# Kernel optimization log

Measured on AMD Instinct MI355X. Metric: run time of the kernel, lower is better.

Reference implementation:

```python
import jax, jax.numpy as jnp
import numpy as np

NEG = -1e6  # matches torch masked value of -1000000.0
EPS = 1e-5


def setup_inputs() -> dict:
    key = jax.random.key(0)
    k1, k2, k3, k4, k5, k6 = jax.random.split(key, 6)
    B, H, L, D = 2, 16, 2048, 128
    BH = B * H
    return {
        "queries": jax.random.normal(k1, (BH, L, D), dtype=jnp.float32),
        "keys": jax.random.normal(k2, (BH, L, D), dtype=jnp.float32),
        "values": jax.random.normal(k3, (BH, L, D), dtype=jnp.float32),
        "q_mult": jax.random.normal(k4, (B, L, D), dtype=jnp.float32),
        "kv_mult": jax.random.normal(k5, (B, L, D), dtype=jnp.float32),
        "valid_lens": jax.random.randint(k6, (BH,), 0, L, dtype=jnp.int64),
        "num_heads": 16,
    }


def reference(queries, keys, values, q_mult, kv_mult, valid_lens, num_heads):
    # queries/keys/values: [BH, L, d]; q_mult/kv_mult: [B, L, d_m]; valid_lens: [BH]
    d = queries.shape[-1]
    Lk = keys.shape[1]
    scale = 1.0 / jnp.sqrt(jnp.asarray(d, dtype=queries.dtype))
    scores = jnp.einsum('bqd,bkd->bqk', queries, keys) * scale  # [BH, Lq, Lk]

    # custom additive multiplicative-interaction term, Frobenius-normalized per batch element
    mult_ = jnp.einsum('bqd,bkd->bqk', q_mult, kv_mult)  # [B, Lq, Lk]
    fro = jnp.sqrt(jnp.sum(mult_ * mult_, axis=(1, 2), keepdims=True))
    mult_ = mult_ / (fro + EPS)
    mult_ = jnp.repeat(mult_, num_heads, axis=0)  # [BH, Lq, Lk]

    # masked softmax over keys: valid_lens is per-(batch*head), broadcast over queries
    key_mask = jnp.arange(Lk)[None, None, :] < valid_lens[:, None, None]  # [BH, 1, Lk]
    scores = jnp.where(key_mask, scores, NEG)
    attn = jax.nn.softmax(scores, axis=-1) + mult_  # after_softmax=True path

    # dropout is identity (p=0 / eval)
    return jnp.einsum('bqk,bkd->bqd', attn, values)
```

## Files before the change

### kernel.cpp

```cpp
#include <hip/hip_runtime.h>


typedef __attribute__((ext_vector_type(8))) __bf16 bf16x8;
typedef __attribute__((ext_vector_type(16))) float f32x16;
typedef __attribute__((ext_vector_type(4))) unsigned int u32x4;

#define DEV static __device__ __forceinline__

constexpr int LL = 2048, DD = 128, BH = 32;
constexpr float SCALE = 0.08838834764831845f;
constexpr float SCALE2 = 0.12752736105f;
constexpr float NEGV = -1e6f;

DEV unsigned pkb(float a, float b) {
  union { __bf16 h[2]; unsigned u; } x;
  x.h[0] = (__bf16)a; x.h[1] = (__bf16)b;
  return x.u;
}
DEV f32x16 mfma32(bf16x8 a, bf16x8 b, f32x16 c) {
  return __builtin_amdgcn_mfma_f32_32x32x16_bf16(a, b, c, 0, 0, 0);
}
DEV void gl16(const void* g, void* l) {
  __builtin_amdgcn_global_load_lds(
      (const __attribute__((address_space(1))) unsigned int*)g,
      (__attribute__((address_space(3))) unsigned int*)l, 16, 0, 0);
}

__global__ __launch_bounds__(256)
void mega_pre(const float* __restrict__ K, const float* __restrict__ V,
              const float* __restrict__ qm, const float* __restrict__ km,
              char* __restrict__ Kb, char* __restrict__ Vt,
              float* __restrict__ Gq, float* __restrict__ Gk,
              float* __restrict__ Mp) {
  __shared__ __align__(16) char smem[16384];
  const int bx = blockIdx.x, tid = threadIdx.x;

  if (bx < 512) {
    float (*skv)[64] = (float(*)[64])smem;
    float (*sv)[128] = (float(*)[128])(smem + 4096);
    int bh = bx & 31, b = bh >> 4, kc = (bx >> 5) & 7, z = (bx >> 8) & 1;
    int l0 = kc * 256;
    int j0 = (tid & 31) * 4, i0 = (tid >> 5) * 8;
    float acc[8][4];
#pragma unroll
    for (int i = 0; i < 8; ++i)
#pragma unroll
      for (int qq = 0; qq < 4; ++qq) acc[i][qq] = 0.f;
    for (int c = 0; c < 16; ++c) {
      __syncthreads();
      {
        int rr = tid >> 4, c4 = (tid & 15) * 4;
        *(float4*)&skv[rr][c4] =
            *(const float4*)(km + (size_t)(b * LL + l0 + c * 16 + rr) * DD + z * 64 + c4);
#pragma unroll
        for (int x = 0; x < 2; ++x) {
          int id2 = x * 256 + tid;
          int r2 = id2 >> 5, c42 = (id2 & 31) * 4;
          *(float4*)&sv[r2][c42] =
              *(const float4*)(V + (size_t)(bh * LL + l0 + c * 16 + r2) * DD + c42);
        }
      }
      __syncthreads();
#pragma unroll
      for (int ll = 0; ll < 16; ++ll) {
        float4 a = *(const float4*)&sv[ll][j0];
        float4 k0 = *(const float4*)&skv[ll][i0];
        float4 k1 = *(const float4*)&skv[ll][i0 + 4];
        float kk[8] = {k0.x, k0.y, k0.z, k0.w, k1.x, k1.y, k1.z, k1.w};
#pragma unroll
        for (int ii = 0; ii < 8; ++ii) {
          acc[ii][0] += kk[ii] * a.x;
          acc[ii][1] += kk[ii] * a.y;
          acc[ii][2] += kk[ii] * a.z;
          acc[ii][3] += kk[ii] * a.w;
        }
      }
    }
    float* dst = Mp + (((size_t)bh * 8 + kc) << 14) + (size_t)(z * 64 + i0) * 128 + j0;
#pragma unroll
    for (int ii = 0; ii < 8; ++ii)
      *(float4*)(dst + (size_t)ii * 128) = *(float4*)&acc[ii][0];

  } else if (bx < 640) {
    float (*s)[128] = (float(*)[128])smem;
    int g = bx - 512;
    int ib = g & 7, lc = (g >> 3) & 3, wb = g >> 5;
    int which = wb >> 1, b = wb & 1;
    const float* A = (which ? km : qm) + (size_t)b * LL * DD;
    float* G = (which ? Gk : Gq) + (size_t)b * DD * DD;
    int i0 = ib * 16 + (tid >> 7) * 8, j = tid & 127;
    int l0 = lc * 512;
    float acc[8];
#pragma unroll
    for (int i = 0; i < 8; ++i) acc[i] = 0.f;
    for (int ch = 0; ch < 16; ++ch) {
      __syncthreads();
#pragma unroll
      for (int i = 0; i < 4; ++i) {
        int c = i * 256 + tid;
        int row = c >> 5, c4 = (c & 31) * 4;
        *(float4*)&s[row][c4] =
            *(const float4*)(A + (size_t)(l0 + ch * 32 + row) * DD + c4);
      }
      __syncthreads();
#pragma unroll
      for (int ll = 0; ll < 32; ++ll) {
        float aj = s[ll][j];
#pragma unroll
        for (int ii = 0; ii < 8; ++ii) acc[ii] += s[ll][i0 + ii] * aj;
      }
    }
#pragma unroll
    for (int ii = 0; ii < 8; ++ii)
      atomicAdd(&G[(size_t)(i0 + ii) * DD + j], acc[ii]);

  } else if (bx < 1664) {
    int pk = bx - 640;
#pragma unroll
    for (int i = 0; i < 4; ++i) {
      int cid = i * 262144 + pk * 256 + tid;
      int h = cid >> 15, k = (cid >> 4) & 2047, c = cid & 15;
      const float* p = K + ((size_t)h * LL + k) * DD + c * 8;
      float4 x0 = *(const float4*)p, x1 = *(const float4*)(p + 4);
      u32x4 v;
      v.x = pkb(x0.x, x0.y); v.y = pkb(x0.z, x0.w);
      v.z = pkb(x1.x, x1.y); v.w = pkb(x1.z, x1.w);
      char* dst = Kb + (((size_t)h * 64 + (k >> 5)) << 13) + ((k & 31) << 8) +
                  ((c ^ (k & 15)) << 4);
      *(u32x4*)dst = v;
    }

  } else {
    float (*sV)[128] = (float(*)[128])smem;
    int pv = bx - 1664;
    int h = pv >> 6, kt = pv & 63;
    const float* src = V + ((size_t)h * LL + kt * 32) * DD;
#pragma unroll
    for (int i = 0; i < 4; ++i) {
      int c = i * 256 + tid;
      int row = c >> 5, c4 = (c & 31) * 4;
      *(float4*)&sV[row][c4] = *(const float4*)(src + (size_t)row * DD + c4);
    }
    __syncthreads();
    char* dstb = Vt + (((size_t)h * 64 + kt) << 13);
#pragma unroll
    for (int i = 0; i < 2; ++i) {
      int cid = i * 256 + tid;
      int f = cid >> 6, l = cid & 63;
      int d = (f >> 1) * 32 + (l & 31);
      int k0 = ((f & 1) * 2 + (l >> 5)) * 8;
      u32x4 v;
      v.x = pkb(sV[k0 + 0][d], sV[k0 + 1][d]);
      v.y = pkb(sV[k0 + 2][d], sV[k0 + 3][d]);
      v.z = pkb(sV[k0 + 4][d], sV[k0 + 5][d]);
      v.w = pkb(sV[k0 + 6][d], sV[k0 + 7][d]);
      *(u32x4*)(dstb + f * 1024 + l * 16) = v;
    }
  }
}

__global__ __launch_bounds__(256)
void k_post(const float* __restrict__ Gq, const float* __restrict__ Gk,
            float* __restrict__ fro, const float* __restrict__ Mp,
            char* __restrict__ MT) {
  int bx = blockIdx.x, tid = threadIdx.x;
  if (bx < 2) {
    int b = bx;
    const float* gq = Gq + (size_t)b * DD * DD;
    const float* gk = Gk + (size_t)b * DD * DD;
    float acc = 0.f;
    for (int i = tid; i < DD * DD; i += 256) acc += gq[i] * gk[i];
#pragma unroll
    for (int m = 32; m; m >>= 1) acc += __shfl_xor(acc, m);
    __shared__ float sbuf[4];
    if ((tid & 63) == 0) sbuf[tid >> 6] = acc;
    __syncthreads();
    if (tid == 0) fro[b] = sqrtf(sbuf[0] + sbuf[1] + sbuf[2] + sbuf[3]);
  } else {
    int g = bx - 2;
    int bh = g >> 2, kq = (g & 3) * 32;
    int k = kq + (tid >> 3), d0 = (tid & 7) * 16;
    float acc[16];
#pragma unroll
    for (int i = 0; i < 16; ++i) acc[i] = 0.f;
#pragma unroll
    for (int s = 0; s < 8; ++s) {
      const float* p = Mp + (((size_t)bh * 8 + s) << 14) + (size_t)k * 128 + d0;
#pragma unroll
      for (int i = 0; i < 4; ++i) {
        float4 v = *(const float4*)(p + i * 4);
        acc[4 * i + 0] += v.x; acc[4 * i + 1] += v.y;
        acc[4 * i + 2] += v.z; acc[4 * i + 3] += v.w;
      }
    }
    char* dst = MT + (size_t)bh * 32768;
#pragma unroll
    for (int j = 0; j < 16; ++j) {
      int d = d0 + j;
      union { __bf16 h; unsigned short u; } cv;
      cv.h = (__bf16)acc[j];
      *(unsigned short*)(dst + d * 256 + (((k >> 3) ^ (d & 15)) << 4) + (k & 7) * 2) = cv.u;
    }
  }
}

__global__ __launch_bounds__(64, 2)
void k_flash1(const char* __restrict__ KbG, const char* __restrict__ VtG,
              const char* __restrict__ MT, const float* __restrict__ fro,
              const float* __restrict__ Qf, const float* __restrict__ qmf,
              const int* __restrict__ vl, float* __restrict__ out) {
  __shared__ __align__(16) char lds[16384];

  const int b_ = blockIdx.x;
  const int xcd = b_ & 7;
  const int j_ = b_ >> 3;
  const int bh = xcd * 4 + (j_ & 3);
  const int qt = j_ >> 2;
  const int b = bh >> 4;
  const int lane = threadIdx.x;
  const int r32 = lane & 31, hi = lane >> 5;
  const int vlen = vl[bh];
  const size_t base = (size_t)bh * LL * DD;
  const int q = qt * 32 + r32;

  bf16x8 qfr[8];
#pragma unroll
  for (int ks = 0; ks < 8; ++ks) {
    const float* p = Qf + base + (size_t)q * DD + ks * 16 + hi * 8;
    float4 x0 = *(const float4*)p, x1 = *(const float4*)(p + 4);
    union { unsigned u[4]; bf16x8 v; } u;
    u.u[0] = pkb(x0.x * SCALE2, x0.y * SCALE2);
    u.u[1] = pkb(x0.z * SCALE2, x0.w * SCALE2);
    u.u[2] = pkb(x1.x * SCALE2, x1.y * SCALE2);
    u.u[3] = pkb(x1.z * SCALE2, x1.w * SCALE2);
    qfr[ks] = u.v;
  }

  f32x16 o[4];
#pragma unroll
  for (int dt = 0; dt < 4; ++dt)
#pragma unroll
    for (int e = 0; e < 16; ++e) o[dt][e] = 0.f;
  float lrun = 0.f;

  int nt = (vlen == 0) ? 64 : ((vlen + 31) >> 5);
  const float mskv = (vlen == 0) ? 0.f : NEGV;

  const char* kb = KbG + (((size_t)bh * 64) << 13);
  const char* vb = VtG + (((size_t)bh * 64) << 13);

  auto stageK = [&](int t, int c2) {
    const char* gk = kb + ((size_t)t << 13) + lane * 16;
    char* lk = lds + c2 * 8192 + lane * 16;
#pragma unroll
    for (int i = 0; i < 8; ++i) gl16(gk + i * 1024, lk + i * 1024);
  };
  auto loadV = [&](int t, u32x4* vr) {
    const char* gv = vb + ((size_t)t << 13) + lane * 16;
#pragma unroll
    for (int f = 0; f < 8; ++f)
      vr[f] = *(const u32x4*)(gv + f * 1024);
  };

  auto compute = [&](const char* Kl, const u32x4* vr, int kbase) {
    f32x16 s0;
#pragma unroll
    for (int e = 0; e < 16; ++e) s0[e] = 0.f;
    __builtin_amdgcn_s_setprio(1);
#pragma unroll
    for (int ks = 0; ks < 8; ++ks) {
      bf16x8 a0 = *(const bf16x8*)(Kl + r32 * 256 + (((2 * ks + hi) ^ (r32 & 15)) << 4));
      s0 = mfma32(a0, qfr[ks], s0);
    }
    __builtin_amdgcn_s_setprio(0);

    if (kbase + 32 > vlen) {
#pragma unroll
      for (int e = 0; e < 16; ++e) {
        int k0 = kbase + (e & 3) + 8 * (e >> 2) + 4 * hi;
        if (k0 >= vlen) s0[e] = mskv;
      }
    }
#pragma unroll
    for (int e = 0; e < 16; ++e) s0[e] = exp2f(s0[e]);
    f32x16 sm = s0;
#pragma unroll
    for (int st = 8; st; st >>= 1)
#pragma unroll
      for (int e = 0; e < st; ++e) sm[e] += sm[e + st];
    lrun += sm[0];

    bf16x8 PA[2];
#pragma unroll
    for (int ks = 0; ks < 2; ++ks) {
      int bb = ks * 8;
      unsigned x1 = pkb(s0[bb + 0], s0[bb + 1]);
      unsigned x2 = pkb(s0[bb + 2], s0[bb + 3]);
      unsigned y1 = pkb(s0[bb + 4], s0[bb + 5]);
      unsigned y2 = pkb(s0[bb + 6], s0[bb + 7]);
      unsigned sx1 = __shfl_xor(x1, 32), sx2 = __shfl_xor(x2, 32);
      unsigned sy1 = __shfl_xor(y1, 32), sy2 = __shfl_xor(y2, 32);
      union { unsigned u[4]; bf16x8 v; } pu;
      pu.u[0] = hi ? sy1 : x1;
      pu.u[1] = hi ? sy2 : x2;
      pu.u[2] = hi ? y1 : sx1;
      pu.u[3] = hi ? y2 : sx2;
      PA[ks] = pu.v;
    }
    __builtin_amdgcn_s_setprio(1);
#pragma unroll
    for (int dt = 0; dt < 4; ++dt)
#pragma unroll
      for (int ks = 0; ks < 2; ++ks) {
        union { u32x4 w; bf16x8 v; } cv;
        cv.w = vr[dt * 2 + ks];
        o[dt] = mfma32(cv.v, PA[ks], o[dt]);
      }
    __builtin_amdgcn_s_setprio(0);
  };

  u32x4 vA[8], vB[8];
  stageK(0, 0);
  loadV(0, vA);
  int t = 0;
  while (true) {
    if (t + 1 < nt) {
      stageK(t + 1, 1); loadV(t + 1, vB);
      asm volatile("s_waitcnt vmcnt(16)" ::: "memory");
    } else {
      asm volatile("s_waitcnt vmcnt(0)" ::: "memory");
    }
    __builtin_amdgcn_sched_barrier(0);
    compute(lds, vA, t * 32);
    if (++t >= nt) break;

    if (t + 1 < nt) {
      stageK(t + 1, 0); loadV(t + 1, vA);
      asm volatile("s_waitcnt vmcnt(16)" ::: "memory");
    } else {
      asm volatile("s_waitcnt vmcnt(0)" ::: "memory");
    }
    __builtin_amdgcn_sched_barrier(0);
    compute(lds + 8192, vB, t * 32);
    if (++t >= nt) break;
  }

  float lt = lrun + __shfl_xor(lrun, 32);
  float inv = 1.f / lt;
#pragma unroll
  for (int dt = 0; dt < 4; ++dt)
#pragma unroll
    for (int e = 0; e < 16; ++e) o[dt][e] *= inv;

  {
    float invf = 1.f / (fro[b] + 1e-5f);
    bf16x8 qb[8];
#pragma unroll
    for (int ks = 0; ks < 8; ++ks) {
      const float* p = qmf + ((size_t)b * LL + q) * DD + ks * 16 + hi * 8;
      float4 x0 = *(const float4*)p, x1 = *(const float4*)(p + 4);
      union { unsigned u[4]; bf16x8 v; } u;
      u.u[0] = pkb(x0.x * invf, x0.y * invf);
      u.u[1] = pkb(x0.z * invf, x0.w * invf);
      u.u[2] = pkb(x1.x * invf, x1.y * invf);
      u.u[3] = pkb(x1.z * invf, x1.w * invf);
      qb[ks] = u.v;
    }
    const char* MTb = MT + (size_t)bh * 32768;
#pragma unroll
    for (int kc = 0; kc < 8; ++kc)
#pragma unroll
      for (int dt = 0; dt < 4; ++dt) {
        bf16x8 av = *(const bf16x8*)(MTb + (dt * 32 + r32) * 256 +
                                     (((2 * kc + hi) ^ (r32 & 15)) << 4));
        o[dt] = mfma32(av, qb[kc], o[dt]);
      }
  }

  float* op = out + base + (size_t)q * DD;
#pragma unroll
  for (int dt = 0; dt < 4; ++dt)
#pragma unroll
    for (int rq = 0; rq < 4; ++rq) {
      float4 v;
      v.x = o[dt][4 * rq + 0];
      v.y = o[dt][4 * rq + 1];
      v.z = o[dt][4 * rq + 2];
      v.w = o[dt][4 * rq + 3];
      *(float4*)(op + dt * 32 + rq * 8 + hi * 4) = v;
    }
}

__global__ __launch_bounds__(128, 2)
void k_flashF(const float* __restrict__ Qf, const float* __restrict__ Kf,
              const float* __restrict__ Vf, const int* __restrict__ vl,
              float* __restrict__ out) {
  __shared__ __align__(16) char lds[16384];
  const int qt = blockIdx.x, bh = blockIdx.y;
  const int tid = threadIdx.x, w = tid >> 6, lane = tid & 63;
  const int r32 = lane & 31, hi = lane >> 5;
  const int vlen = vl[bh];
  const size_t base = (size_t)bh * LL * DD;
  const int q = qt * 64 + w * 32 + r32;

  bf16x8 qfr[8];
#pragma unroll
  for (int ks = 0; ks < 8; ++ks) {
    const float* p = Qf + base + (size_t)q * DD + ks * 16 + hi * 8;
    float4 x0 = *(const float4*)p, x1 = *(const float4*)(p + 4);
    union { unsigned u[4]; bf16x8 v; } u;
    u.u[0] = pkb(x0.x * SCALE, x0.y * SCALE);
    u.u[1] = pkb(x0.z * SCALE, x0.w * SCALE);
    u.u[2] = pkb(x1.x * SCALE, x1.y * SCALE);
    u.u[3] = pkb(x1.z * SCALE, x1.w * SCALE);
    qfr[ks] = u.v;
  }

  f32x16 o[4];
#pragma unroll
  for (int dt = 0; dt < 4; ++dt)
#pragma unroll
    for (int e = 0; e < 16; ++e) o[dt][e] = 0.f;
  float mrun = -3e38f, lrun = 0.f;
  int nt = (vlen == 0) ? 64 : ((vlen + 31) >> 5);

  char* Kl = lds;
  char* Vl = lds + 8192;
  for (int t = 0; t < nt; ++t) {
    int kbase = t * 32;
    __syncthreads();
#pragma unroll
    for (int i = 0; i < 4; ++i) {
      int c = i * 128 + tid;
      int kk = c >> 4, sl = c & 15;
      const float* p = Kf + base + (size_t)(kbase + kk) * DD + sl * 8;
      float4 x0 = *(const float4*)p, x1 = *(const float4*)(p + 4);
      u32x4 v;
      v.x = pkb(x0.x, x0.y); v.y = pkb(x0.z, x0.w);
      v.z = pkb(x1.x, x1.y); v.w = pkb(x1.z, x1.w);
      *(u32x4*)(Kl + (kk << 8) + ((sl ^ (kk & 15)) << 4)) = v;
    }
#pragma unroll
    for (int i = 0; i < 4; ++i) {
      int c = i * 128 + tid;
      int d = c >> 2, kk8 = c & 3;
      float t0[8];
#pragma unroll
      for (int j = 0; j < 8; ++j)
        t0[j] = Vf[base + (size_t)(kbase + kk8 * 8 + j) * DD + d];
      u32x4 v;
      v.x = pkb(t0[0], t0[1]); v.y = pkb(t0[2], t0[3]);
      v.z = pkb(t0[4], t0[5]); v.w = pkb(t0[6], t0[7]);
      *(u32x4*)(Vl + d * 64 + ((kk8 ^ ((d >> 1) & 3)) << 4)) = v;
    }
    __syncthreads();

    f32x16 s0;
#pragma unroll
    for (int e = 0; e < 16; ++e) s0[e] = 0.f;
#pragma unroll
    for (int ks = 0; ks < 8; ++ks) {
      bf16x8 a0 = *(const bf16x8*)(Kl + r32 * 256 + (((2 * ks + hi) ^ (r32 & 15)) << 4));
      s0 = mfma32(a0, qfr[ks], s0);
    }
    if (kbase + 32 > vlen) {
#pragma unroll
      for (int e = 0; e < 16; ++e) {
        int k0 = kbase + (e & 3) + 8 * (e >> 2) + 4 * hi;
        if (k0 >= vlen) s0[e] = NEGV;
      }
    }
    f32x16 mx = s0;
#pragma unroll
    for (int st = 8; st; st >>= 1)
#pragma unroll
      for (int e = 0; e < st; ++e) mx[e] = fmaxf(mx[e], mx[e + st]);
    float pm = fmaxf(mx[0], __shfl_xor(mx[0], 32));
    if (!__all(pm <= mrun + 8.f)) {
      float mn = fmaxf(mrun, pm);
      float al = __expf(mrun - mn);
      lrun *= al;
#pragma unroll
      for (int dt = 0; dt < 4; ++dt)
#pragma unroll
        for (int e = 0; e < 16; ++e) o[dt][e] *= al;
      mrun = mn;
    }
#pragma unroll
    for (int e = 0; e < 16; ++e) s0[e] = __expf(s0[e] - mrun);
    f32x16 sm = s0;
#pragma unroll
    for (int st = 8; st; st >>= 1)
#pragma unroll
      for (int e = 0; e < st; ++e) sm[e] += sm[e + st];
    lrun += sm[0];

    bf16x8 PA[2];
#pragma unroll
    for (int ks = 0; ks < 2; ++ks) {
      int bb = ks * 8;
      unsigned x1 = pkb(s0[bb + 0], s0[bb + 1]);
      unsigned x2 = pkb(s0[bb + 2], s0[bb + 3]);
      unsigned y1 = pkb(s0[bb + 4], s0[bb + 5]);
      unsigned y2 = pkb(s0[bb + 6], s0[bb + 7]);
      unsigned sx1 = __shfl_xor(x1, 32), sx2 = __shfl_xor(x2, 32);
      unsigned sy1 = __shfl_xor(y1, 32), sy2 = __shfl_xor(y2, 32);
      union { unsigned u[4]; bf16x8 v; } pu;
      pu.u[0] = hi ? sy1 : x1;
      pu.u[1] = hi ? sy2 : x2;
      pu.u[2] = hi ? y1 : sx1;
      pu.u[3] = hi ? y2 : sx2;
      PA[ks] = pu.v;
    }
#pragma unroll
    for (int dt = 0; dt < 4; ++dt)
#pragma unroll
      for (int ks = 0; ks < 2; ++ks) {
        bf16x8 av = *(const bf16x8*)(Vl + (dt * 32 + r32) * 64 +
                                     (((2 * ks + hi) ^ ((r32 >> 1) & 3)) << 4));
        o[dt] = mfma32(av, PA[ks], o[dt]);
      }
    __syncthreads();
  }

  float lt = lrun + __shfl_xor(lrun, 32);
  float inv = 1.f / lt;
  float* op = out + base + (size_t)q * DD;
#pragma unroll
  for (int dt = 0; dt < 4; ++dt)
#pragma unroll
    for (int rq = 0; rq < 4; ++rq) {
      float4 v;
      v.x = o[dt][4 * rq + 0] * inv;
      v.y = o[dt][4 * rq + 1] * inv;
      v.z = o[dt][4 * rq + 2] * inv;
      v.w = o[dt][4 * rq + 3] * inv;
      *(float4*)(op + dt * 32 + rq * 8 + hi * 4) = v;
    }
}

__global__ void k_gram(const float* __restrict__ qm, const float* __restrict__ km,
                       float* __restrict__ Gq, float* __restrict__ Gk) {
  int which = blockIdx.z >> 1, b = blockIdx.z & 1;
  const float* A = (which ? km : qm) + (size_t)b * LL * DD;
  float* G = (which ? Gk : Gq) + (size_t)b * DD * DD;
  int i0 = blockIdx.x * 8;
  int l0 = blockIdx.y * 512;
  __shared__ float s[32][128];
  float acc[8];
#pragma unroll
  for (int i = 0; i < 8; ++i) acc[i] = 0.f;
  for (int ch = 0; ch < 16; ++ch) {
    __syncthreads();
    for (int rr = 0; rr < 32; ++rr)
      s[rr][threadIdx.x] = A[(size_t)(l0 + ch * 32 + rr) * DD + threadIdx.x];
    __syncthreads();
    for (int ll = 0; ll < 32; ++ll) {
      float aj = s[ll][threadIdx.x];
#pragma unroll
      for (int ii = 0; ii < 8; ++ii) acc[ii] += s[ll][i0 + ii] * aj;
    }
  }
#pragma unroll
  for (int ii = 0; ii < 8; ++ii)
    atomicAdd(&G[(size_t)(i0 + ii) * DD + threadIdx.x], acc[ii]);
}

__global__ void k_fro(const float* __restrict__ Gq, const float* __restrict__ Gk,
                      float* __restrict__ fro) {
  int b = blockIdx.x;
  const float* gq = Gq + (size_t)b * DD * DD;
  const float* gk = Gk + (size_t)b * DD * DD;
  float acc = 0.f;
  for (int i = threadIdx.x; i < DD * DD; i += 256) acc += gq[i] * gk[i];
#pragma unroll
  for (int m = 32; m; m >>= 1) acc += __shfl_xor(acc, m);
  __shared__ float sbuf[4];
  if ((threadIdx.x & 63) == 0) sbuf[threadIdx.x >> 6] = acc;
  __syncthreads();
  if (threadIdx.x == 0) fro[b] = sqrtf(sbuf[0] + sbuf[1] + sbuf[2] + sbuf[3]);
}

__global__ void k_M_atomic(const float* __restrict__ km, const float* __restrict__ Vf,
                           float* __restrict__ M) {
  int bh = blockIdx.x, b = bh >> 4;
  int l0 = blockIdx.y * 128;
  __shared__ float skv[16][128];
  __shared__ float sv[16][128];
  int j0 = (threadIdx.x & 31) * 4;
  int i0 = (threadIdx.x >> 5) * 16;
  float acc[16][4];
#pragma unroll
  for (int i = 0; i < 16; ++i)
#pragma unroll
    for (int qq = 0; qq < 4; ++qq) acc[i][qq] = 0.f;
  for (int c = 0; c < 8; ++c) {
    __syncthreads();
    for (int x = 0; x < 8; ++x) {
      int idx = x * 256 + threadIdx.x;
      int rr = idx >> 7, cc = idx & 127;
      skv[rr][cc] = km[(size_t)(b * LL + l0 + c * 16 + rr) * DD + cc];
      sv[rr][cc] = Vf[(size_t)(bh * LL + l0 + c * 16 + rr) * DD + cc];
    }
    __syncthreads();
    for (int ll = 0; ll < 16; ++ll) {
      float a0 = sv[ll][j0], a1 = sv[ll][j0 + 1];
      float a2 = sv[ll][j0 + 2], a3 = sv[ll][j0 + 3];
#pragma unroll
      for (int ii = 0; ii < 16; ++ii) {
        float kv = skv[ll][i0 + ii];
        acc[ii][0] += kv * a0;
        acc[ii][1] += kv * a1;
        acc[ii][2] += kv * a2;
        acc[ii][3] += kv * a3;
      }
    }
  }
#pragma unroll
  for (int ii = 0; ii < 16; ++ii)
#pragma unroll
    for (int qq = 0; qq < 4; ++qq)
      atomicAdd(&M[(size_t)bh * DD * DD + (size_t)(i0 + ii) * DD + j0 + qq],
                acc[ii][qq]);
}

__global__ void k_multadd(const float* __restrict__ qm, const float* __restrict__ M,
                          const float* __restrict__ fro, float* __restrict__ out) {
  int bh = blockIdx.y, b = bh >> 4;
  int l = blockIdx.x * 128 + (threadIdx.x & 127);
  int dh = (threadIdx.x >> 7) * 64;
  float inv = 1.0f / (fro[b] + 1e-5f);
  const float* qrow = qm + ((size_t)b * LL + l) * DD;
  const float* Mb = M + (size_t)bh * DD * DD + dh;
  float acc[64];
#pragma unroll
  for (int i = 0; i < 64; ++i) acc[i] = 0.f;
  for (int k = 0; k < 128; ++k) {
    float qv = qrow[k];
    const float4* m4 = (const float4*)(Mb + (size_t)k * DD);
#pragma unroll
    for (int i = 0; i < 16; ++i) {
      float4 mm = m4[i];
      acc[4 * i + 0] += qv * mm.x;
      acc[4 * i + 1] += qv * mm.y;
      acc[4 * i + 2] += qv * mm.z;
      acc[4 * i + 3] += qv * mm.w;
    }
  }
  float* op = out + ((size_t)bh * LL + l) * DD + dh;
#pragma unroll
  for (int i = 0; i < 16; ++i) {
    float4 ov = ((float4*)op)[i];
    ov.x += acc[4 * i + 0] * inv;
    ov.y += acc[4 * i + 1] * inv;
    ov.z += acc[4 * i + 2] * inv;
    ov.w += acc[4 * i + 3] * inv;
    ((float4*)op)[i] = ov;
  }
}

extern "C" void kernel_launch(void* const* d_in, const int* in_sizes, int n_in,
                              void* d_out, int out_size, void* d_ws, size_t ws_size,
                              hipStream_t stream) {
  (void)in_sizes; (void)n_in; (void)out_size;
  const float* Q = (const float*)d_in[0];
  const float* K = (const float*)d_in[1];
  const float* V = (const float*)d_in[2];
  const float* qm = (const float*)d_in[3];
  const float* km = (const float*)d_in[4];
  const int* vl = (const int*)d_in[5];
  float* out = (float*)d_out;

  char* ws = (char*)d_ws;
  const size_t off_Gq = 0;
  const size_t off_Gk = 131072;
  const size_t off_fro = 262144;
  const size_t off_MT = 294912;
  const size_t off_Kb = off_MT + 1048576;
  const size_t szb = (size_t)BH * LL * DD * 2;
  const size_t off_Vt = off_Kb + szb;
  const size_t off_end = off_Vt + szb;
  bool fits = ws_size >= off_end;

  float* Gq = (float*)(ws + off_Gq);
  float* Gk = (float*)(ws + off_Gk);
  float* fro = (float*)(ws + off_fro);
  char* MT = ws + off_MT;

  if (fits) {
    float* Mp = (float*)d_out;
    hipMemsetAsync(ws, 0, off_fro + 256, stream);
    mega_pre<<<3712, 256, 0, stream>>>(K, V, qm, km, ws + off_Kb, ws + off_Vt,
                                       Gq, Gk, Mp);
    k_post<<<130, 256, 0, stream>>>(Gq, Gk, fro, Mp, MT);
    k_flash1<<<2048, 64, 0, stream>>>(ws + off_Kb, ws + off_Vt, MT, fro,
                                      Q, qm, vl, out);
  } else {
    float* Mw = (float*)(ws + off_MT);
    hipMemsetAsync(ws, 0, off_MT + 2097152, stream);
    k_gram<<<dim3(16, 4, 4), 128, 0, stream>>>(qm, km, Gq, Gk);
    k_fro<<<2, 256, 0, stream>>>(Gq, Gk, fro);
    k_flashF<<<dim3(32, 32), 128, 0, stream>>>(Q, K, V, vl, out);
    k_M_atomic<<<dim3(32, 16), 256, 0, stream>>>(km, V, Mw);
    k_multadd<<<dim3(16, 32), 256, 0, stream>>>(qm, Mw, fro, out);
  }
}
```

Baseline: 183.5 us.

## Split key tiles across two waves per query block with LDS reduction

The flash kernel now runs two wavefronts per 32-query block. Each wave takes alternate key tiles with its own double-buffered LDS region, and the partial outputs and row sums are combined through shared memory before the final normalization and multiplicative-term epilogue. This cuts the serial key-loop length per wave for long valid lengths and adds parallelism. The cost is a larger LDS footprint, an extra reduction and barrier, and loss of the XCD-aware block remapping in favour of a plain 2D grid.

Result: faster. 161.4 us (-12.1%).

```diff
diff --git a/kernel.cpp b/kernel.cpp
--- a/kernel.cpp
+++ b/kernel.cpp
@@ -204,24 +204,20 @@
   }
 }
 
-__global__ __launch_bounds__(64, 2)
-void k_flash1(const char* __restrict__ KbG, const char* __restrict__ VtG,
+__global__ __launch_bounds__(128, 2)
+void k_flash2(const char* __restrict__ KbG, const char* __restrict__ VtG,
               const char* __restrict__ MT, const float* __restrict__ fro,
               const float* __restrict__ Qf, const float* __restrict__ qmf,
               const int* __restrict__ vl, float* __restrict__ out) {
-  __shared__ __align__(16) char lds[16384];
-
-  const int b_ = blockIdx.x;
-  const int xcd = b_ & 7;
-  const int j_ = b_ >> 3;
-  const int bh = xcd * 4 + (j_ & 3);
-  const int qt = j_ >> 2;
-  const int b = bh >> 4;
-  const int lane = threadIdx.x;
+  __shared__ __align__(16) char lds[33024];
+
+  const int qt = blockIdx.x, bh = blockIdx.y, b = bh >> 4;
+  const int tid = threadIdx.x, w = tid >> 6, lane = tid & 63;
   const int r32 = lane & 31, hi = lane >> 5;
   const int vlen = vl[bh];
   const size_t base = (size_t)bh * LL * DD;
   const int q = qt * 32 + r32;
+  char* ldsW = lds + w * 16384;
 
   bf16x8 qfr[8];
 #pragma unroll
@@ -251,7 +247,7 @@
 
   auto stageK = [&](int t, int c2) {
     const char* gk = kb + ((size_t)t << 13) + lane * 16;
-    char* lk = lds + c2 * 8192 + lane * 16;
+    char* lk = ldsW + c2 * 8192 + lane * 16;
 #pragma unroll
     for (int i = 0; i < 8; ++i) gl16(gk + i * 1024, lk + i * 1024);
   };
@@ -319,38 +315,57 @@
     __builtin_amdgcn_s_setprio(0);
   };
 
-  u32x4 vA[8], vB[8];
-  stageK(0, 0);
-  loadV(0, vA);
-  int t = 0;
-  while (true) {
-    if (t + 1 < nt) {
-      stageK(t + 1, 1); loadV(t + 1, vB);
-      asm volatile("s_waitcnt vmcnt(16)" ::: "memory");
-    } else {
-      asm volatile("s_waitcnt vmcnt(0)" ::: "memory");
-    }
-    __builtin_amdgcn_sched_barrier(0);
-    compute(lds, vA, t * 32);
-    if (++t >= nt) break;
-
-    if (t + 1 < nt) {
-      stageK(t + 1, 0); loadV(t + 1, vA);
-      asm volatile("s_waitcnt vmcnt(16)" ::: "memory");
-    } else {
-      asm volatile("s_waitcnt vmcnt(0)" ::: "memory");
-    }
-    __builtin_amdgcn_sched_barrier(0);
-    compute(lds + 8192, vB, t * 32);
-    if (++t >= nt) break;
-  }
-
-  float lt = lrun + __shfl_xor(lrun, 32);
+  {
+    u32x4 vA[8], vB[8];
+    int t = w;
+    if (t < nt) {
+      stageK(t, 0);
+      loadV(t, vA);
+      while (true) {
+        if (t + 2 < nt) {
+          stageK(t + 2, 1); loadV(t + 2, vB);
+          asm volatile("s_waitcnt vmcnt(16)" ::: "memory");
+        } else {
+          asm volatile("s_waitcnt vmcnt(0)" ::: "memory");
+        }
+        __builtin_amdgcn_sched_barrier(0);
+        compute(ldsW, vA, t * 32);
+        t += 2; if (t >= nt) break;
+
+        if (t + 2 < nt) {
+          stageK(t + 2, 0); loadV(t + 2, vA);
+          asm volatile("s_waitcnt vmcnt(16)" ::: "memory");
+        } else {
+          asm volatile("s_waitcnt vmcnt(0)" ::: "memory");
+        }
+        __builtin_amdgcn_sched_barrier(0);
+        compute(ldsW + 8192, vB, t * 32);
+        t += 2; if (t >= nt) break;
+      }
+    }
+  }
+
+  float ltw = lrun + __shfl_xor(lrun, 32);
+  float* oshare = (float*)(lds + 16384);
+  float* lshare = (float*)(lds + 32768);
+  if (w == 1) {
+#pragma unroll
+    for (int dt = 0; dt < 4; ++dt)
+#pragma unroll
+      for (int e = 0; e < 16; ++e)
+        oshare[(dt * 16 + e) * 64 + lane] = o[dt][e];
+    if (hi == 0) lshare[r32] = ltw;
+  }
+  __syncthreads();
+  if (w == 1) return;
+
+  float lt = ltw + lshare[r32];
   float inv = 1.f / lt;
 #pragma unroll
   for (int dt = 0; dt < 4; ++dt)
 #pragma unroll
-    for (int e = 0; e < 16; ++e) o[dt][e] *= inv;
+    for (int e = 0; e < 16; ++e)
+      o[dt][e] = (o[dt][e] + oshare[(dt * 16 + e) * 64 + lane]) * inv;
 
   {
     float invf = 1.f / (fro[b] + 1e-5f);
@@ -693,8 +708,8 @@
     mega_pre<<<3712, 256, 0, stream>>>(K, V, qm, km, ws + off_Kb, ws + off_Vt,
                                        Gq, Gk, Mp);
     k_post<<<130, 256, 0, stream>>>(Gq, Gk, fro, Mp, MT);
-    k_flash1<<<2048, 64, 0, stream>>>(ws + off_Kb, ws + off_Vt, MT, fro,
-                                      Q, qm, vl, out);
+    k_flash2<<<dim3(64, 32), 128, 0, stream>>>(ws + off_Kb, ws + off_Vt, MT, fro,
+                                               Q, qm, vl, out);
   } else {
     float* Mw = (float*)(ws + off_MT);
     hipMemsetAsync(ws, 0, off_MT + 2097152, stream);
```
